# Optimization experiments

Hardware: AMD Instinct MI355X
Metric: run time of the kernel (lower is better)

Reference implementation:

```python
import jax, jax.numpy as jnp
import numpy as np

N_HEADS = 8
TANH_CLIP = 10.0
NEG_INF = -jnp.inf


def _one_step(step_ctx, fixed_ctx, gK, gV, logitK, W_step, W_out, visited):
    # step_ctx: (B,2D)  fixed_ctx: (B,D)  gK,gV: (H,B,N,dk)  logitK: (B,N,D)  visited: (B,N) bool
    H, B, N, dk = gK.shape
    D = fixed_ctx.shape[-1]
    # query = fixed context + projected step context
    q = fixed_ctx + step_ctx @ W_step                      # (B,D)
    qh = q.reshape(B, H, dk).transpose(1, 0, 2)            # (H,B,dk)
    compat = jnp.einsum('hbk,hbnk->hbn', qh, gK) / jnp.sqrt(jnp.float32(dk))
    compat = jnp.where(visited[None], NEG_INF, compat)     # mask_inner
    attn = jax.nn.softmax(compat, axis=-1)                 # (H,B,N)
    heads = jnp.einsum('hbn,hbnk->hbk', attn, gV)          # (H,B,dk)
    glimpse = heads.transpose(1, 0, 2).reshape(B, D) @ W_out  # (B,D) project_out
    logits = jnp.einsum('bd,bnd->bn', glimpse, logitK) / jnp.sqrt(jnp.float32(D))
    logits = TANH_CLIP * jnp.tanh(logits)                  # tanh clipping
    logits = jnp.where(visited, NEG_INF, logits)           # mask_logits
    return jax.nn.log_softmax(logits, axis=-1)             # (B,N)


def setup_inputs() -> dict:
    key = jax.random.key(0)
    ks = jax.random.split(key, 6)
    B, N, D = 128, 1000, 128
    return {
        'embeddings': jax.random.normal(ks[0], (B, N, D), jnp.float32),
        'W_node': jax.random.normal(ks[1], (D, 3 * D), jnp.float32) / np.sqrt(D).astype(np.float32),
        'W_fixed': jax.random.normal(ks[2], (D, D), jnp.float32) / np.sqrt(D).astype(np.float32),
        'W_step': jax.random.normal(ks[3], (2 * D, D), jnp.float32) / np.sqrt(2 * D).astype(np.float32),
        'W_out': jax.random.normal(ks[4], (D, D), jnp.float32) / np.sqrt(D).astype(np.float32),
        'W_placeholder': jax.random.uniform(ks[5], (2 * D,), jnp.float32, -1.0, 1.0),
        'n_steps': 64,
    }


def reference(embeddings, W_node, W_fixed, W_step, W_out, W_placeholder, n_steps):
    B, N, D = embeddings.shape
    H, dk = N_HEADS, D // N_HEADS
    # _precompute: project node embeddings to glimpse K/V and logit K (no bias)
    kvq = embeddings @ W_node                              # (B,N,3D)
    gK, gV, lK = jnp.split(kvq, 3, axis=-1)
    gK = gK.reshape(B, N, H, dk).transpose(2, 0, 1, 3)     # (H,B,N,dk)
    gV = gV.reshape(B, N, H, dk).transpose(2, 0, 1, 3)
    fixed_ctx = jnp.mean(embeddings, axis=1) @ W_fixed     # (B,D) graph embedding context

    visited0 = jnp.zeros((B, N), dtype=bool)
    # step 0: TSP uses learned placeholder as step context
    ctx0 = jnp.broadcast_to(W_placeholder, (B, 2 * D))
    logp0 = _one_step(ctx0, fixed_ctx, gK, gV, lK, W_step, W_out, visited0)
    sel0 = jnp.argmax(logp0, axis=-1)                      # greedy decode (B,)
    visited1 = visited0.at[jnp.arange(B), sel0].set(True)
    first_emb = jnp.take_along_axis(embeddings, sel0[:, None, None], axis=1)[:, 0]  # (B,D)

    def body(carry, _):
        visited, prev_emb = carry
        step_ctx = jnp.concatenate([first_emb, prev_emb], axis=-1)  # (B,2D)
        logp = _one_step(step_ctx, fixed_ctx, gK, gV, lK, W_step, W_out, visited)
        sel = jnp.argmax(logp, axis=-1)
        visited = visited.at[jnp.arange(visited.shape[0]), sel].set(True)
        prev = jnp.take_along_axis(embeddings, sel[:, None, None], axis=1)[:, 0]
        return (visited, prev), (logp, sel)

    (_, _), (logps, sels) = jax.lax.scan(body, (visited1, first_emb), None, length=n_steps - 1)
    log_p = jnp.concatenate([logp0[:, None], logps.transpose(1, 0, 2)], axis=1)  # (B,S,N)
    pi = jnp.concatenate([sel0[:, None], sels.T], axis=1)                        # (B,S)
    return log_p, pi
```

## Files before the change

kernel.cpp:

```cpp
#include <hip/hip_runtime.h>
#include <math.h>

#define B 128
#define N 1000
#define NP 1024
#define D 128
#define H 8
#define DK 16
#define STEPS 64
#define NEG_INF (-INFINITY)
#define OUT_NEG (-1.0e30f)


__global__ __launch_bounds__(256)
void precompute_kernel(const float* __restrict__ emb, const float* __restrict__ Wn,
                       float* __restrict__ gK, float* __restrict__ gV,
                       float* __restrict__ lKt) {
  const int rt = blockIdx.x;
  const int cc = blockIdx.y;
  const int t  = threadIdx.x;
  const int tx = t & 15, ty = t >> 4;
  __shared__ float4 wL[64 * 32];

  float acc[8][8];
#pragma unroll
  for (int i = 0; i < 8; ++i)
#pragma unroll
    for (int j = 0; j < 8; ++j) acc[i][j] = 0.f;

  const float4* Wn4 = (const float4*)Wn;
  const float* ebase = emb + (size_t)(rt * 128 + ty * 8) * 128;

  for (int kk = 0; kk < 2; ++kk) {
    __syncthreads();
    for (int idx = t; idx < 64 * 32; idx += 256) {
      int dl = idx >> 5, c4 = idx & 31;
      wL[dl * 32 + c4] = Wn4[(size_t)(kk * 64 + dl) * 96 + cc * 32 + c4];
    }
    __syncthreads();
    for (int dl = 0; dl < 64; dl += 4) {
      float4 e4[8];
#pragma unroll
      for (int i = 0; i < 8; ++i)
        e4[i] = *(const float4*)(ebase + (size_t)i * 128 + kk * 64 + dl);
#pragma unroll
      for (int dd = 0; dd < 4; ++dd) {
        float4 w0 = wL[(dl + dd) * 32 + tx * 2];
        float4 w1 = wL[(dl + dd) * 32 + tx * 2 + 1];
        float w_[8] = {w0.x, w0.y, w0.z, w0.w, w1.x, w1.y, w1.z, w1.w};
        float e_[8] = {
          dd == 0 ? e4[0].x : dd == 1 ? e4[0].y : dd == 2 ? e4[0].z : e4[0].w,
          dd == 0 ? e4[1].x : dd == 1 ? e4[1].y : dd == 2 ? e4[1].z : e4[1].w,
          dd == 0 ? e4[2].x : dd == 1 ? e4[2].y : dd == 2 ? e4[2].z : e4[2].w,
          dd == 0 ? e4[3].x : dd == 1 ? e4[3].y : dd == 2 ? e4[3].z : e4[3].w,
          dd == 0 ? e4[4].x : dd == 1 ? e4[4].y : dd == 2 ? e4[4].z : e4[4].w,
          dd == 0 ? e4[5].x : dd == 1 ? e4[5].y : dd == 2 ? e4[5].z : e4[5].w,
          dd == 0 ? e4[6].x : dd == 1 ? e4[6].y : dd == 2 ? e4[6].z : e4[6].w,
          dd == 0 ? e4[7].x : dd == 1 ? e4[7].y : dd == 2 ? e4[7].z : e4[7].w};
#pragma unroll
        for (int i = 0; i < 8; ++i)
#pragma unroll
          for (int j = 0; j < 8; ++j) acc[i][j] += e_[i] * w_[j];
      }
    }
  }

  const int lc = tx * 8;
#pragma unroll
  for (int i = 0; i < 8; ++i) {
    int row = rt * 128 + ty * 8 + i;
    int b = row / 1000;
    int n = row - b * 1000;
    if (cc < 2) {
      int h = lc >> 4, k = lc & 15;
      float* dst = (cc == 0 ? gK : gV) + (((size_t)(h * B + b)) * N + n) * DK + k;
      *(float4*)dst       = make_float4(acc[i][0], acc[i][1], acc[i][2], acc[i][3]);
      *(float4*)(dst + 4) = make_float4(acc[i][4], acc[i][5], acc[i][6], acc[i][7]);
    } else {
#pragma unroll
      for (int j = 0; j < 8; ++j)
        lKt[((size_t)b * D + lc + j) * NP + n] = acc[i][j];
    }
  }
}

__global__ __launch_bounds__(256)
void fixed_ctx_kernel(const float* __restrict__ emb, const float* __restrict__ Wf,
                      float* __restrict__ fixed_ctx) {
  const int b = blockIdx.x;
  const int t = threadIdx.x;
  const int d = t & 127, half = t >> 7;
  __shared__ float part[256];
  __shared__ float meanL[128];
  float s = 0.f;
  for (int n = half; n < N; n += 2) s += emb[((size_t)b * N + n) * D + d];
  part[t] = s;
  __syncthreads();
  if (t < 128) meanL[t] = (part[t] + part[t + 128]) * (1.0f / (float)N);
  __syncthreads();
  if (t < 128) {
    float a = 0.f;
    for (int k = 0; k < 128; ++k) a += meanL[k] * Wf[k * 128 + t];
    fixed_ctx[b * 128 + t] = a;
  }
}

__global__ __launch_bounds__(256)
void glimpse_kernel(const float* __restrict__ gK, const float* __restrict__ gV,
                    const float* __restrict__ fixed_ctx, const float* __restrict__ W_step,
                    const float* __restrict__ Wp, const float* __restrict__ first_emb,
                    const float* __restrict__ prev_emb, const int* __restrict__ visited,
                    float* __restrict__ heads, int step) {
  const int b = blockIdx.x & (B - 1);
  const int h = blockIdx.x >> 7;
  const int t = threadIdx.x;
  const int lane = t & 63, wid = t >> 6;
  __shared__ float qred[16][17];
  __shared__ float qL[16];
  __shared__ float redA[4];
  __shared__ float hred[4][16];

  {
    int k = t & 15, part = t >> 4;
    float s = 0.f;
    for (int jj = 0; jj < 16; ++jj) {
      int i = part + jj * 16;
      float ctx;
      if (step == 0) ctx = Wp[i];
      else ctx = (i < D) ? first_emb[b * D + i] : prev_emb[b * D + i - D];
      s += ctx * W_step[i * D + h * DK + k];
    }
    qred[part][k] = s;
  }
  __syncthreads();
  if (t < 16) {
    float s = fixed_ctx[b * D + h * DK + t];
    for (int p = 0; p < 16; ++p) s += qred[p][t];
    qL[t] = s * 0.25f;
  }
  __syncthreads();
  float q[16];
#pragma unroll
  for (int k = 0; k < 16; ++k) q[k] = qL[k];

  float c[4];
  const float4* gK4 = (const float4*)(gK + (((size_t)(h * B + b)) * N) * DK);
#pragma unroll
  for (int j = 0; j < 4; ++j) {
    int n = t + j * 256;
    float cv = NEG_INF;
    if (n < N && visited[b * NP + n] == 0) {
      float4 a0 = gK4[n * 4 + 0], a1 = gK4[n * 4 + 1];
      float4 a2 = gK4[n * 4 + 2], a3 = gK4[n * 4 + 3];
      cv = a0.x * q[0] + a0.y * q[1] + a0.z * q[2] + a0.w * q[3]
         + a1.x * q[4] + a1.y * q[5] + a1.z * q[6] + a1.w * q[7]
         + a2.x * q[8] + a2.y * q[9] + a2.z * q[10] + a2.w * q[11]
         + a3.x * q[12] + a3.y * q[13] + a3.z * q[14] + a3.w * q[15];
    }
    c[j] = cv;
  }

  float m = fmaxf(fmaxf(c[0], c[1]), fmaxf(c[2], c[3]));
#pragma unroll
  for (int off = 32; off >= 1; off >>= 1) m = fmaxf(m, __shfl_xor(m, off));
  if (lane == 0) redA[wid] = m;
  __syncthreads();
  m = fmaxf(fmaxf(redA[0], redA[1]), fmaxf(redA[2], redA[3]));

  float p[4];
  float s = 0.f;
#pragma unroll
  for (int j = 0; j < 4; ++j) {
    p[j] = (c[j] == NEG_INF) ? 0.f : expf(c[j] - m);
    s += p[j];
  }
#pragma unroll
  for (int off = 32; off >= 1; off >>= 1) s += __shfl_xor(s, off);
  __syncthreads();
  if (lane == 0) redA[wid] = s;
  __syncthreads();
  s = redA[0] + redA[1] + redA[2] + redA[3];

  float hacc[16];
#pragma unroll
  for (int k = 0; k < 16; ++k) hacc[k] = 0.f;
  const float4* gV4 = (const float4*)(gV + (((size_t)(h * B + b)) * N) * DK);
#pragma unroll
  for (int j = 0; j < 4; ++j) {
    int n = t + j * 256;
    if (n < N && p[j] > 0.f) {
      float4 a0 = gV4[n * 4 + 0], a1 = gV4[n * 4 + 1];
      float4 a2 = gV4[n * 4 + 2], a3 = gV4[n * 4 + 3];
      hacc[0] += p[j] * a0.x;  hacc[1] += p[j] * a0.y;
      hacc[2] += p[j] * a0.z;  hacc[3] += p[j] * a0.w;
      hacc[4] += p[j] * a1.x;  hacc[5] += p[j] * a1.y;
      hacc[6] += p[j] * a1.z;  hacc[7] += p[j] * a1.w;
      hacc[8] += p[j] * a2.x;  hacc[9] += p[j] * a2.y;
      hacc[10] += p[j] * a2.z; hacc[11] += p[j] * a2.w;
      hacc[12] += p[j] * a3.x; hacc[13] += p[j] * a3.y;
      hacc[14] += p[j] * a3.z; hacc[15] += p[j] * a3.w;
    }
  }
#pragma unroll
  for (int k = 0; k < 16; ++k) {
    float v = hacc[k];
#pragma unroll
    for (int off = 32; off >= 1; off >>= 1) v += __shfl_xor(v, off);
    hacc[k] = v;
  }
  if (lane == 0) {
#pragma unroll
    for (int k = 0; k < 16; ++k) hred[wid][k] = hacc[k];
  }
  __syncthreads();
  if (t < 16) {
    float v = hred[0][t] + hred[1][t] + hred[2][t] + hred[3][t];
    heads[b * D + h * DK + t] = v / s;
  }
}

__global__ __launch_bounds__(256)
void logits_kernel(const float* __restrict__ lKt, const float* __restrict__ heads,
                   const float* __restrict__ W_out, const float* __restrict__ emb,
                   int* __restrict__ visited, float* __restrict__ first_emb,
                   float* __restrict__ prev_emb, float* __restrict__ out, int step) {
  const int b = blockIdx.x;
  const int t = threadIdx.x;
  const int lane = t & 63, wid = t >> 6;
  __shared__ float hL[128];
  __shared__ float gl[128];
  __shared__ float redV[4];
  __shared__ int   redI[4];
  __shared__ float mS;
  __shared__ int   selS;

  if (t < 128) hL[t] = heads[b * D + t];
  __syncthreads();
  if (t < 128) {
    float a = 0.f;
    for (int k = 0; k < 128; ++k) a += hL[k] * W_out[k * 128 + t];
    gl[t] = a;
  }
  __syncthreads();

  float acc[4] = {0.f, 0.f, 0.f, 0.f};
  const float4* lk4 = (const float4*)(lKt + (size_t)b * D * NP);
  for (int d = 0; d < 128; ++d) {
    float g = gl[d];
    float4 v = lk4[d * (NP / 4) + t];
    acc[0] += g * v.x; acc[1] += g * v.y; acc[2] += g * v.z; acc[3] += g * v.w;
  }
  const float sqrtD = 11.313708498984761f;
  float lv[4];
  int ok[4];
#pragma unroll
  for (int j = 0; j < 4; ++j) {
    int n = t * 4 + j;
    int valid = (n < N) && (visited[b * NP + n] == 0);
    float l = 10.f * tanhf(acc[j] / sqrtD);
    lv[j] = valid ? l : NEG_INF;
    ok[j] = valid;
  }

  float bv = lv[0];
  int bi = t * 4;
#pragma unroll
  for (int j = 1; j < 4; ++j)
    if (lv[j] > bv) { bv = lv[j]; bi = t * 4 + j; }
#pragma unroll
  for (int off = 32; off >= 1; off >>= 1) {
    float ov = __shfl_xor(bv, off);
    int oi = __shfl_xor(bi, off);
    if (ov > bv || (ov == bv && oi < bi)) { bv = ov; bi = oi; }
  }
  if (lane == 0) { redV[wid] = bv; redI[wid] = bi; }
  __syncthreads();
  if (t == 0) {
    float mv = redV[0]; int mi = redI[0];
    for (int w = 1; w < 4; ++w)
      if (redV[w] > mv || (redV[w] == mv && redI[w] < mi)) { mv = redV[w]; mi = redI[w]; }
    mS = mv; selS = mi;
  }
  __syncthreads();
  const float m = mS;

  float se = 0.f;
#pragma unroll
  for (int j = 0; j < 4; ++j) if (ok[j]) se += expf(lv[j] - m);
#pragma unroll
  for (int off = 32; off >= 1; off >>= 1) se += __shfl_xor(se, off);
  __syncthreads();
  if (lane == 0) redV[wid] = se;
  __syncthreads();
  se = redV[0] + redV[1] + redV[2] + redV[3];
  const float lse = m + logf(se);

  if (t < 250) {
    float4 o;
    o.x = ok[0] ? (lv[0] - lse) : OUT_NEG;
    o.y = ok[1] ? (lv[1] - lse) : OUT_NEG;
    o.z = ok[2] ? (lv[2] - lse) : OUT_NEG;
    o.w = ok[3] ? (lv[3] - lse) : OUT_NEG;
    ((float4*)(out + ((size_t)b * STEPS + step) * N))[t] = o;
  }

  const int sel = selS;
  if (t == 0) {
    out[(size_t)B * STEPS * N + b * STEPS + step] = (float)sel;
    visited[b * NP + sel] = 1;
  }
  if (t < 128) {
    float e = emb[((size_t)b * N + sel) * D + t];
    prev_emb[b * D + t] = e;
    if (step == 0) first_emb[b * D + t] = e;
  }
}

extern "C" void kernel_launch(void* const* d_in, const int* in_sizes, int n_in,
                              void* d_out, int out_size, void* d_ws, size_t ws_size,
                              hipStream_t stream) {
  (void)in_sizes; (void)n_in; (void)out_size; (void)ws_size;
  const float* emb     = (const float*)d_in[0];
  const float* W_node  = (const float*)d_in[1];
  const float* W_fixed = (const float*)d_in[2];
  const float* W_step  = (const float*)d_in[3];
  const float* W_out   = (const float*)d_in[4];
  const float* Wp      = (const float*)d_in[5];
  float* out = (float*)d_out;
  float* ws  = (float*)d_ws;

  float* gK        = ws;
  float* gV        = gK + (size_t)H * B * N * DK;
  float* lKt       = gV + (size_t)H * B * N * DK;
  float* fixed_ctx = lKt + (size_t)B * D * NP;
  float* heads     = fixed_ctx + B * D;
  float* first_emb = heads + B * D;
  float* prev_emb  = first_emb + B * D;
  int*   visited   = (int*)(prev_emb + B * D);

  hipMemsetAsync(visited, 0, (size_t)B * NP * sizeof(int), stream);
  precompute_kernel<<<dim3(1000, 3), 256, 0, stream>>>(emb, W_node, gK, gV, lKt);
  fixed_ctx_kernel<<<B, 256, 0, stream>>>(emb, W_fixed, fixed_ctx);
  for (int s = 0; s < STEPS; ++s) {
    glimpse_kernel<<<H * B, 256, 0, stream>>>(gK, gV, fixed_ctx, W_step, Wp,
                                              first_emb, prev_emb, visited, heads, s);
    logits_kernel<<<B, 256, 0, stream>>>(lKt, heads, W_out, emb, visited,
                                         first_emb, prev_emb, out, s);
  }
}
```

Before: 2.828 ms.

## Fold glimpse K/V projections into query and output, attending directly over embeddings

Drops the precomputed per-head gK/gV tensors. The query is instead projected through W_node's K slice (q·Wk^T), so compatibilities come straight from the raw embeddings. The attention-weighted embedding sums are projected through W_node's V slice afterwards in the logits kernel. This removes materialising and re-reading two large (H,B,N,dk) tensors each step and cuts the precompute work to a third, at the cost of fewer, larger glimpse blocks (B blocks of 512 threads with about 36KB of shared memory) and some extra small matmuls per step.

```diff
diff --git a/kernel.cpp b/kernel.cpp
--- a/kernel.cpp
+++ b/kernel.cpp
@@ -13,11 +13,9 @@
 
 
 __global__ __launch_bounds__(256)
-void precompute_kernel(const float* __restrict__ emb, const float* __restrict__ Wn,
-                       float* __restrict__ gK, float* __restrict__ gV,
-                       float* __restrict__ lKt) {
+void precompute_lkt(const float* __restrict__ emb, const float* __restrict__ Wn,
+                    float* __restrict__ lKt) {
   const int rt = blockIdx.x;
-  const int cc = blockIdx.y;
   const int t  = threadIdx.x;
   const int tx = t & 15, ty = t >> 4;
   __shared__ float4 wL[64 * 32];
@@ -35,7 +33,7 @@
     __syncthreads();
     for (int idx = t; idx < 64 * 32; idx += 256) {
       int dl = idx >> 5, c4 = idx & 31;
-      wL[dl * 32 + c4] = Wn4[(size_t)(kk * 64 + dl) * 96 + cc * 32 + c4];
+      wL[dl * 32 + c4] = Wn4[(size_t)(kk * 64 + dl) * 96 + 64 + c4];
     }
     __syncthreads();
     for (int dl = 0; dl < 64; dl += 4) {
@@ -65,22 +63,14 @@
     }
   }
 
-  const int lc = tx * 8;
 #pragma unroll
   for (int i = 0; i < 8; ++i) {
     int row = rt * 128 + ty * 8 + i;
     int b = row / 1000;
     int n = row - b * 1000;
-    if (cc < 2) {
-      int h = lc >> 4, k = lc & 15;
-      float* dst = (cc == 0 ? gK : gV) + (((size_t)(h * B + b)) * N + n) * DK + k;
-      *(float4*)dst       = make_float4(acc[i][0], acc[i][1], acc[i][2], acc[i][3]);
-      *(float4*)(dst + 4) = make_float4(acc[i][4], acc[i][5], acc[i][6], acc[i][7]);
-    } else {
-#pragma unroll
-      for (int j = 0; j < 8; ++j)
-        lKt[((size_t)b * D + lc + j) * NP + n] = acc[i][j];
-    }
+#pragma unroll
+    for (int j = 0; j < 8; ++j)
+      lKt[((size_t)b * D + tx * 8 + j) * NP + n] = acc[i][j];
   }
 }
 
@@ -105,140 +95,180 @@
   }
 }
 
+__global__ __launch_bounds__(512)
+void glimpse_emb(const float* __restrict__ emb, const float* __restrict__ Wn,
+                 const float* __restrict__ Wstep, const float* __restrict__ Wp,
+                 const float* __restrict__ fixed_ctx,
+                 const float* __restrict__ first_emb, const float* __restrict__ prev_emb,
+                 const int* __restrict__ visited,
+                 float* __restrict__ wePg, int step) {
+  const int b = blockIdx.x;
+  const int t = threadIdx.x;
+  const int lane = t & 63, wv = t >> 6;
+  const int r = (lane >> 4) & 3, c = lane & 15;
+
+  __shared__ float ctxL[256];
+  __shared__ float qL[128];
+  __shared__ float qkL[8][128];
+  __shared__ float cL[8][1024];
+  __shared__ float sH[8];
+
+  if (t < 256) {
+    float v;
+    if (step == 0) v = Wp[t];
+    else v = (t < 128) ? first_emb[b * D + t] : prev_emb[b * D + (t - 128)];
+    ctxL[t] = v;
+  }
+  __syncthreads();
+
+  if (t < 128) {
+    float a = fixed_ctx[b * D + t];
+    for (int i = 0; i < 256; ++i) a += ctxL[i] * Wstep[i * D + t];
+    qL[t] = a;
+  }
+  __syncthreads();
+
+  {
+    int d = t >> 2, h0 = (t & 3) * 2;
+#pragma unroll
+    for (int u = 0; u < 2; ++u) {
+      int hh = h0 + u;
+      float a = 0.f;
+#pragma unroll
+      for (int k = 0; k < 16; ++k) a += qL[hh * 16 + k] * Wn[(size_t)d * 384 + hh * 16 + k];
+      qkL[hh][d] = a * 0.25f;
+    }
+  }
+  __syncthreads();
+
+  const float4* emb4 = (const float4*)emb;
+
+  {
+    float qkr[8][8];
+#pragma unroll
+    for (int h = 0; h < 8; ++h)
+#pragma unroll
+      for (int j = 0; j < 8; ++j) qkr[h][j] = qkL[h][c * 8 + j];
+
+    for (int it = 0; it < 32; ++it) {
+      int n = it * 32 + wv * 4 + r;
+      float4 e0 = make_float4(0.f, 0.f, 0.f, 0.f), e1 = e0;
+      if (n < N) {
+        e0 = emb4[((size_t)b * N + n) * 32 + c * 2];
+        e1 = emb4[((size_t)b * N + n) * 32 + c * 2 + 1];
+      }
+      float s[8];
+#pragma unroll
+      for (int h = 0; h < 8; ++h) {
+        s[h] = qkr[h][0] * e0.x + qkr[h][1] * e0.y + qkr[h][2] * e0.z + qkr[h][3] * e0.w
+             + qkr[h][4] * e1.x + qkr[h][5] * e1.y + qkr[h][6] * e1.z + qkr[h][7] * e1.w;
+      }
+#pragma unroll
+      for (int off = 1; off <= 8; off <<= 1)
+#pragma unroll
+        for (int h = 0; h < 8; ++h) s[h] += __shfl_xor(s[h], off);
+      if (c == 0) {
+        bool vis = (n >= N) || (visited[b * NP + n] != 0);
+#pragma unroll
+        for (int h = 0; h < 8; ++h) cL[h][n] = vis ? NEG_INF : s[h];
+      }
+    }
+  }
+  __syncthreads();
+
+  {
+    int h = wv;
+    float vals[16];
+    float m = NEG_INF;
+#pragma unroll
+    for (int j = 0; j < 16; ++j) { vals[j] = cL[h][lane + j * 64]; m = fmaxf(m, vals[j]); }
+#pragma unroll
+    for (int off = 1; off <= 32; off <<= 1) m = fmaxf(m, __shfl_xor(m, off));
+    float ssum = 0.f;
+#pragma unroll
+    for (int j = 0; j < 16; ++j) {
+      float p = (vals[j] == NEG_INF) ? 0.f : expf(vals[j] - m);
+      cL[h][lane + j * 64] = p;
+      ssum += p;
+    }
+#pragma unroll
+    for (int off = 1; off <= 32; off <<= 1) ssum += __shfl_xor(ssum, off);
+    if (lane == 0) sH[h] = ssum;
+  }
+  __syncthreads();
+
+  float wa[8][8];
+#pragma unroll
+  for (int h = 0; h < 8; ++h)
+#pragma unroll
+    for (int j = 0; j < 8; ++j) wa[h][j] = 0.f;
+
+  for (int it = 0; it < 32; ++it) {
+    int n = it * 32 + wv * 4 + r;
+    if (n < N) {
+      float4 e0 = emb4[((size_t)b * N + n) * 32 + c * 2];
+      float4 e1 = emb4[((size_t)b * N + n) * 32 + c * 2 + 1];
+#pragma unroll
+      for (int h = 0; h < 8; ++h) {
+        float p = cL[h][n];
+        wa[h][0] += p * e0.x; wa[h][1] += p * e0.y;
+        wa[h][2] += p * e0.z; wa[h][3] += p * e0.w;
+        wa[h][4] += p * e1.x; wa[h][5] += p * e1.y;
+        wa[h][6] += p * e1.z; wa[h][7] += p * e1.w;
+      }
+    }
+  }
+#pragma unroll
+  for (int h = 0; h < 8; ++h)
+#pragma unroll
+    for (int j = 0; j < 8; ++j) {
+      wa[h][j] += __shfl_xor(wa[h][j], 16);
+      wa[h][j] += __shfl_xor(wa[h][j], 32);
+    }
+  if (lane < 16) {
+#pragma unroll
+    for (int h = 0; h < 8; ++h) {
+      float inv = 1.0f / sH[h];
+      float* dst = wePg + ((size_t)(b * 8 + wv) * 8 + h) * 128 + lane * 8;
+      *(float4*)dst       = make_float4(wa[h][0] * inv, wa[h][1] * inv, wa[h][2] * inv, wa[h][3] * inv);
+      *(float4*)(dst + 4) = make_float4(wa[h][4] * inv, wa[h][5] * inv, wa[h][6] * inv, wa[h][7] * inv);
+    }
+  }
+}
+
 __global__ __launch_bounds__(256)
-void glimpse_kernel(const float* __restrict__ gK, const float* __restrict__ gV,
-                    const float* __restrict__ fixed_ctx, const float* __restrict__ W_step,
-                    const float* __restrict__ Wp, const float* __restrict__ first_emb,
-                    const float* __restrict__ prev_emb, const int* __restrict__ visited,
-                    float* __restrict__ heads, int step) {
-  const int b = blockIdx.x & (B - 1);
-  const int h = blockIdx.x >> 7;
-  const int t = threadIdx.x;
-  const int lane = t & 63, wid = t >> 6;
-  __shared__ float qred[16][17];
-  __shared__ float qL[16];
-  __shared__ float redA[4];
-  __shared__ float hred[4][16];
-
-  {
-    int k = t & 15, part = t >> 4;
-    float s = 0.f;
-    for (int jj = 0; jj < 16; ++jj) {
-      int i = part + jj * 16;
-      float ctx;
-      if (step == 0) ctx = Wp[i];
-      else ctx = (i < D) ? first_emb[b * D + i] : prev_emb[b * D + i - D];
-      s += ctx * W_step[i * D + h * DK + k];
-    }
-    qred[part][k] = s;
-  }
-  __syncthreads();
-  if (t < 16) {
-    float s = fixed_ctx[b * D + h * DK + t];
-    for (int p = 0; p < 16; ++p) s += qred[p][t];
-    qL[t] = s * 0.25f;
-  }
-  __syncthreads();
-  float q[16];
-#pragma unroll
-  for (int k = 0; k < 16; ++k) q[k] = qL[k];
-
-  float c[4];
-  const float4* gK4 = (const float4*)(gK + (((size_t)(h * B + b)) * N) * DK);
-#pragma unroll
-  for (int j = 0; j < 4; ++j) {
-    int n = t + j * 256;
-    float cv = NEG_INF;
-    if (n < N && visited[b * NP + n] == 0) {
-      float4 a0 = gK4[n * 4 + 0], a1 = gK4[n * 4 + 1];
-      float4 a2 = gK4[n * 4 + 2], a3 = gK4[n * 4 + 3];
-      cv = a0.x * q[0] + a0.y * q[1] + a0.z * q[2] + a0.w * q[3]
-         + a1.x * q[4] + a1.y * q[5] + a1.z * q[6] + a1.w * q[7]
-         + a2.x * q[8] + a2.y * q[9] + a2.z * q[10] + a2.w * q[11]
-         + a3.x * q[12] + a3.y * q[13] + a3.z * q[14] + a3.w * q[15];
-    }
-    c[j] = cv;
-  }
-
-  float m = fmaxf(fmaxf(c[0], c[1]), fmaxf(c[2], c[3]));
-#pragma unroll
-  for (int off = 32; off >= 1; off >>= 1) m = fmaxf(m, __shfl_xor(m, off));
-  if (lane == 0) redA[wid] = m;
-  __syncthreads();
-  m = fmaxf(fmaxf(redA[0], redA[1]), fmaxf(redA[2], redA[3]));
-
-  float p[4];
-  float s = 0.f;
-#pragma unroll
-  for (int j = 0; j < 4; ++j) {
-    p[j] = (c[j] == NEG_INF) ? 0.f : expf(c[j] - m);
-    s += p[j];
-  }
-#pragma unroll
-  for (int off = 32; off >= 1; off >>= 1) s += __shfl_xor(s, off);
-  __syncthreads();
-  if (lane == 0) redA[wid] = s;
-  __syncthreads();
-  s = redA[0] + redA[1] + redA[2] + redA[3];
-
-  float hacc[16];
-#pragma unroll
-  for (int k = 0; k < 16; ++k) hacc[k] = 0.f;
-  const float4* gV4 = (const float4*)(gV + (((size_t)(h * B + b)) * N) * DK);
-#pragma unroll
-  for (int j = 0; j < 4; ++j) {
-    int n = t + j * 256;
-    if (n < N && p[j] > 0.f) {
-      float4 a0 = gV4[n * 4 + 0], a1 = gV4[n * 4 + 1];
-      float4 a2 = gV4[n * 4 + 2], a3 = gV4[n * 4 + 3];
-      hacc[0] += p[j] * a0.x;  hacc[1] += p[j] * a0.y;
-      hacc[2] += p[j] * a0.z;  hacc[3] += p[j] * a0.w;
-      hacc[4] += p[j] * a1.x;  hacc[5] += p[j] * a1.y;
-      hacc[6] += p[j] * a1.z;  hacc[7] += p[j] * a1.w;
-      hacc[8] += p[j] * a2.x;  hacc[9] += p[j] * a2.y;
-      hacc[10] += p[j] * a2.z; hacc[11] += p[j] * a2.w;
-      hacc[12] += p[j] * a3.x; hacc[13] += p[j] * a3.y;
-      hacc[14] += p[j] * a3.z; hacc[15] += p[j] * a3.w;
-    }
-  }
-#pragma unroll
-  for (int k = 0; k < 16; ++k) {
-    float v = hacc[k];
-#pragma unroll
-    for (int off = 32; off >= 1; off >>= 1) v += __shfl_xor(v, off);
-    hacc[k] = v;
-  }
-  if (lane == 0) {
-#pragma unroll
-    for (int k = 0; k < 16; ++k) hred[wid][k] = hacc[k];
-  }
-  __syncthreads();
-  if (t < 16) {
-    float v = hred[0][t] + hred[1][t] + hred[2][t] + hred[3][t];
-    heads[b * D + h * DK + t] = v / s;
-  }
-}
-
-__global__ __launch_bounds__(256)
-void logits_kernel(const float* __restrict__ lKt, const float* __restrict__ heads,
-                   const float* __restrict__ W_out, const float* __restrict__ emb,
+void logits_kernel(const float* __restrict__ lKt, const float* __restrict__ wePg,
+                   const float* __restrict__ Wn, const float* __restrict__ W_out,
+                   const float* __restrict__ emb,
                    int* __restrict__ visited, float* __restrict__ first_emb,
                    float* __restrict__ prev_emb, float* __restrict__ out, int step) {
   const int b = blockIdx.x;
   const int t = threadIdx.x;
   const int lane = t & 63, wid = t >> 6;
-  __shared__ float hL[128];
+  __shared__ float weN[8][128];
+  __shared__ float headsL[128];
   __shared__ float gl[128];
   __shared__ float redV[4];
   __shared__ int   redI[4];
   __shared__ float mS;
   __shared__ int   selS;
 
-  if (t < 128) hL[t] = heads[b * D + t];
-  __syncthreads();
-  if (t < 128) {
+  for (int idx = t; idx < 1024; idx += 256) {
     float a = 0.f;
-    for (int k = 0; k < 128; ++k) a += hL[k] * W_out[k * 128 + t];
+    for (int w = 0; w < 8; ++w) a += wePg[(size_t)(b * 8 + w) * 1024 + idx];
+    weN[idx >> 7][idx & 127] = a;
+  }
+  __syncthreads();
+  if (t < 128) {
+    int h = t >> 4, k = t & 15;
+    float a = 0.f;
+    for (int d = 0; d < 128; ++d) a += weN[h][d] * Wn[(size_t)d * 384 + 128 + h * 16 + k];
+    headsL[t] = a;
+  }
+  __syncthreads();
+  if (t < 128) {
+    float a = 0.f;
+    for (int k = 0; k < 128; ++k) a += headsL[k] * W_out[k * 128 + t];
     gl[t] = a;
   }
   __syncthreads();
@@ -329,22 +359,20 @@
   float* out = (float*)d_out;
   float* ws  = (float*)d_ws;
 
-  float* gK        = ws;
-  float* gV        = gK + (size_t)H * B * N * DK;
-  float* lKt       = gV + (size_t)H * B * N * DK;
-  float* fixed_ctx = lKt + (size_t)B * D * NP;
-  float* heads     = fixed_ctx + B * D;
-  float* first_emb = heads + B * D;
-  float* prev_emb  = first_emb + B * D;
-  int*   visited   = (int*)(prev_emb + B * D);
+  float* fixed_ctx = ws;
+  float* lKt       = fixed_ctx + (size_t)B * D;
+  float* wePg      = lKt + (size_t)B * D * NP;
+  float* first_emb = wePg + (size_t)B * 8 * 8 * 128;
+  float* prev_emb  = first_emb + (size_t)B * D;
+  int*   visited   = (int*)(prev_emb + (size_t)B * D);
 
   hipMemsetAsync(visited, 0, (size_t)B * NP * sizeof(int), stream);
-  precompute_kernel<<<dim3(1000, 3), 256, 0, stream>>>(emb, W_node, gK, gV, lKt);
+  precompute_lkt<<<1000, 256, 0, stream>>>(emb, W_node, lKt);
   fixed_ctx_kernel<<<B, 256, 0, stream>>>(emb, W_fixed, fixed_ctx);
   for (int s = 0; s < STEPS; ++s) {
-    glimpse_kernel<<<H * B, 256, 0, stream>>>(gK, gV, fixed_ctx, W_step, Wp,
-                                              first_emb, prev_emb, visited, heads, s);
-    logits_kernel<<<B, 256, 0, stream>>>(lKt, heads, W_out, emb, visited,
+    glimpse_emb<<<B, 512, 0, stream>>>(emb, W_node, W_step, Wp, fixed_ctx,
+                                       first_emb, prev_emb, visited, wePg, s);
+    logits_kernel<<<B, 256, 0, stream>>>(lKt, wePg, W_node, W_out, emb, visited,
                                          first_emb, prev_emb, out, s);
   }
 }
```

New measurement: 5.917 ms. 2.09x slower.
